# Optimization experiments

Hardware: AMD Instinct MI355X
Metric: run time of the kernel (lower is better)

Reference implementation:

```python
import jax, jax.numpy as jnp
import numpy as np

N, E, D, L, BOT = 50000, 800000, 64, 5, 15
EPS = 1e-5  # BatchNorm eps (torch default)
GATE = 0.01


def _bn(x, g, b):
    # training-mode BatchNorm1d over the node (batch) axis, biased variance
    m = jnp.mean(x, axis=0)
    v = jnp.mean((x - m) ** 2, axis=0)
    return (x - m) * jax.lax.rsqrt(v + EPS) * g + b


def _adapter(x, w1, b1, w2, b2, g, b):
    # Linear(D->BOT) -> ReLU -> Linear(BOT->D) -> BatchNorm1d
    h = jax.nn.relu(x @ w1 + b1)
    return _bn(h @ w2 + b2, g, b)


def setup_inputs() -> dict:
    key = jax.random.key(0)
    ks = jax.random.split(key, 8)
    x = jax.random.normal(ks[0], (N, D), dtype=jnp.float32)
    edge_index = jax.random.randint(ks[1], (2, E), 0, N, dtype=jnp.int32)
    # per-layer conv Linear weights
    W = jax.random.normal(ks[2], (L, D, D), dtype=jnp.float32) * 0.05
    b = jnp.zeros((L, D), dtype=jnp.float32)
    # per-layer output BatchNorm
    bn_g = jnp.ones((L, D), dtype=jnp.float32)
    bn_b = jnp.zeros((L, D), dtype=jnp.float32)
    # adapter branches: [prompt_num=2, L, ...] (random init so grads are nontrivial)
    pw1 = jax.random.normal(ks[3], (2, L, D, BOT), dtype=jnp.float32) * 0.1
    pb1 = jnp.zeros((2, L, BOT), dtype=jnp.float32)
    pw2 = jax.random.normal(ks[4], (2, L, BOT, D), dtype=jnp.float32) * 0.1
    pb2 = jnp.zeros((2, L, D), dtype=jnp.float32)
    pbn_g = jnp.ones((2, L, D), dtype=jnp.float32)
    pbn_b = jnp.zeros((2, L, D), dtype=jnp.float32)
    gating = jnp.full((2, L, 1), GATE, dtype=jnp.float32)
    return dict(x=x, edge_index=edge_index, W=W, b=b, bn_g=bn_g, bn_b=bn_b,
                pw1=pw1, pb1=pb1, pw2=pw2, pb2=pb2, pbn_g=pbn_g, pbn_b=pbn_b,
                gating=gating)


def reference(x, edge_index, W, b, bn_g, bn_b, pw1, pb1, pw2, pb2, pbn_g, pbn_b, gating):
    src, dst = edge_index[0], edge_index[1]
    h = x
    for l in range(L):
        # mess: sum-aggregate neighbor features (scatter-add over dst)
        x_aggr = jax.ops.segment_sum(h[src], dst, num_segments=N)  # [N, D]
        # conv: Linear on aggregated messages
        h_mlp = x_aggr @ W[l] + b[l]
        hn = _bn(h_mlp, bn_g[l], bn_b[l])
        # adapter branch 0 on layer input, branch 1 on aggregated messages
        hn = hn + _adapter(h, pw1[0, l], pb1[0, l], pw2[0, l], pb2[0, l], pbn_g[0, l], pbn_b[0, l]) * gating[0, l]
        hn = hn + _adapter(x_aggr, pw1[1, l], pb1[1, l], pw2[1, l], pb2[1, l], pbn_g[1, l], pbn_b[1, l]) * gating[1, l]
        if l < L - 1:
            hn = jax.nn.relu(hn)
        # dropout with drop_ratio=0 is a no-op
        h = hn
    return h
```

## Files before the change

kernel.cpp:

```cpp
#include <hip/hip_runtime.h>
#include <hip/hip_fp16.h>

#define DIM 64
#define BOT 15
#define NLAYERS 5
#define BN_EPS 1e-5f
#define ROWS 64
#define ROWS_FB 32
#define BKT_SHIFT 8
#define NSTRIPE 4

__device__ inline void fma4(float4& acc, const float4& a, float s) {
    acc.x = fmaf(a.x, s, acc.x); acc.y = fmaf(a.y, s, acc.y);
    acc.z = fmaf(a.z, s, acc.z); acc.w = fmaf(a.w, s, acc.w);
}
__device__ inline void add4(float4& acc, const float4& a) {
    acc.x += a.x; acc.y += a.y; acc.z += a.z; acc.w += a.w;
}
__device__ inline void fma4sq(float4& acc, const float4& a) {
    acc.x = fmaf(a.x, a.x, acc.x); acc.y = fmaf(a.y, a.y, acc.y);
    acc.z = fmaf(a.z, a.z, acc.z); acc.w = fmaf(a.w, a.w, acc.w);
}
__device__ inline void wavered4(float4& v) {
    v.x += __shfl_xor(v.x, 16); v.y += __shfl_xor(v.y, 16);
    v.z += __shfl_xor(v.z, 16); v.w += __shfl_xor(v.w, 16);
    v.x += __shfl_xor(v.x, 32); v.y += __shfl_xor(v.y, 32);
    v.z += __shfl_xor(v.z, 32); v.w += __shfl_xor(v.w, 32);
}


__global__ __launch_bounds__(256) void hist_k(const int* __restrict__ dst,
                                              int* __restrict__ deg, int E) {
    int e = blockIdx.x * blockDim.x + threadIdx.x;
    if (e < E) atomicAdd(&deg[dst[e]], 1);
}

__global__ __launch_bounds__(1024) void scan_part_k(const int* __restrict__ deg,
                                                    int* __restrict__ excl,
                                                    int* __restrict__ bsum, int n) {
    __shared__ int buf[1024];
    int t = threadIdx.x;
    int idx = blockIdx.x * 1024 + t;
    int v = (idx < n) ? deg[idx] : 0;
    buf[t] = v;
    __syncthreads();
    for (int off = 1; off < 1024; off <<= 1) {
        int x = (t >= off) ? buf[t - off] : 0;
        __syncthreads();
        buf[t] += x;
        __syncthreads();
    }
    if (idx < n) excl[idx] = buf[t] - v;
    if (t == 0) bsum[blockIdx.x] = buf[1023];
}

__global__ __launch_bounds__(1024) void scan_top_k(const int* __restrict__ bsum,
                                                   int* __restrict__ boff, int nb,
                                                   int* __restrict__ row_ptr, int n) {
    __shared__ int buf[1024];
    int t = threadIdx.x;
    int v = (t < nb) ? bsum[t] : 0;
    buf[t] = v;
    __syncthreads();
    for (int off = 1; off < 1024; off <<= 1) {
        int x = (t >= off) ? buf[t - off] : 0;
        __syncthreads();
        buf[t] += x;
        __syncthreads();
    }
    if (t < nb) boff[t] = buf[t] - v;
    if (t == 1023) row_ptr[n] = buf[1023];
}

__global__ __launch_bounds__(256) void scan_add_k(int* __restrict__ row_ptr,
                                                  const int* __restrict__ boff,
                                                  int* __restrict__ deg,
                                                  int* __restrict__ bcur, int n) {
    int i = blockIdx.x * blockDim.x + threadIdx.x;
    if (i < n) {
        int v = row_ptr[i] + boff[i >> 10];
        row_ptr[i] = v;
        deg[i] = v;
        if ((i & 255) == 0) bcur[i >> BKT_SHIFT] = v;
    }
}

__global__ __launch_bounds__(256) void scatter_k(const int* __restrict__ src,
                                                 const int* __restrict__ dst,
                                                 int* __restrict__ cursor,
                                                 int* __restrict__ csr, int E) {
    int e = blockIdx.x * blockDim.x + threadIdx.x;
    if (e < E) {
        int p = atomicAdd(&cursor[dst[e]], 1);
        csr[p] = src[e];
    }
}

__global__ __launch_bounds__(256) void part_k(const int* __restrict__ src,
                                              const int* __restrict__ dst,
                                              int* __restrict__ bcur,
                                              int2* __restrict__ part, int E) {
    __shared__ int hist[256];
    __shared__ int cur[256];
    int t = threadIdx.x;
    int base = blockIdx.x * 2048;
    hist[t] = 0;
    __syncthreads();
    int2 ed[8];
    int bk[8];
    #pragma unroll
    for (int k = 0; k < 8; k++) {
        int i = base + k * 256 + t;
        if (i < E) {
            ed[k].x = src[i];
            ed[k].y = dst[i];
            bk[k] = ed[k].y >> BKT_SHIFT;
            atomicAdd(&hist[bk[k]], 1);
        } else bk[k] = -1;
    }
    __syncthreads();
    int h = hist[t];
    if (h > 0) cur[t] = atomicAdd(&bcur[t], h);
    __syncthreads();
    #pragma unroll
    for (int k = 0; k < 8; k++) {
        if (bk[k] >= 0) {
            int p = atomicAdd(&cur[bk[k]], 1);
            part[p] = ed[k];
        }
    }
}

__global__ __launch_bounds__(256) void bscat_k(const int2* __restrict__ part,
                                               const int* __restrict__ row_ptr,
                                               int* __restrict__ cursor,
                                               int* __restrict__ csr, int n) {
    int b = blockIdx.x;
    int lo = row_ptr[b << BKT_SHIFT];
    int hiN = (b + 1) << BKT_SHIFT;
    int hi = row_ptr[hiN < n ? hiN : n];
    for (int i = lo + (int)threadIdx.x; i < hi; i += 256) {
        int2 e = part[i];
        int p = atomicAdd(&cursor[e.y], 1);
        csr[p] = e.x;
    }
}


__global__ __launch_bounds__(256) void tohalf_k(const float* __restrict__ x,
                                                __half* __restrict__ hh, int n4) {
    int i = blockIdx.x * blockDim.x + threadIdx.x;
    if (i >= n4) return;
    float4 v = *(const float4*)&x[(size_t)i * 4];
    __half2 a = __floats2half2_rn(v.x, v.y);
    __half2 b = __floats2half2_rn(v.z, v.w);
    uint2 pk;
    pk.x = *(unsigned int*)&a;
    pk.y = *(unsigned int*)&b;
    *(uint2*)&hh[(size_t)i * 4] = pk;
}


__global__ __launch_bounds__(256) void aggr_h_k(const __half* __restrict__ hh,
                                                const int* __restrict__ row_ptr,
                                                const int* __restrict__ csr,
                                                float* __restrict__ out, int n) {
    int gid = blockIdx.x * blockDim.x + threadIdx.x;
    int node = gid >> 6;
    int lane = threadIdx.x & 63;
    if (node >= n) return;
    int j = lane >> 3, q = lane & 7;
    int s = row_ptr[node], e = row_ptr[node + 1];
    float acc[8] = {0.f, 0.f, 0.f, 0.f, 0.f, 0.f, 0.f, 0.f};
    #pragma unroll 2
    for (int i = s; i < e; i += 8) {
        int ii = i + j;
        if (ii < e) {
            int idx = csr[ii];
            uint4 raw = *(const uint4*)&hh[(size_t)idx * DIM + q * 8];
            const __half2* hp = (const __half2*)&raw;
            #pragma unroll
            for (int k = 0; k < 4; k++) {
                acc[2 * k]     += __low2float(hp[k]);
                acc[2 * k + 1] += __high2float(hp[k]);
            }
        }
    }
    #pragma unroll
    for (int off = 8; off <= 32; off <<= 1) {
        #pragma unroll
        for (int k = 0; k < 8; k++) acc[k] += __shfl_xor(acc[k], off);
    }
    if (lane < 8) {
        float4 a = {acc[0], acc[1], acc[2], acc[3]};
        float4 b = {acc[4], acc[5], acc[6], acc[7]};
        *(float4*)&out[(size_t)node * DIM + q * 8] = a;
        *(float4*)&out[(size_t)node * DIM + q * 8 + 4] = b;
    }
}

__global__ __launch_bounds__(256) void aggr_k(const float* __restrict__ h,
                                              const int* __restrict__ row_ptr,
                                              const int* __restrict__ csr,
                                              float* __restrict__ out, int n) {
    int gid = blockIdx.x * blockDim.x + threadIdx.x;
    int node = gid >> 6;
    int lane = threadIdx.x & 63;
    if (node >= n) return;
    int j = lane >> 4, q = lane & 15;
    int s = row_ptr[node], e = row_ptr[node + 1];
    float4 acc = {0.f, 0.f, 0.f, 0.f};
    #pragma unroll 4
    for (int i = s; i < e; i += 4) {
        int ii = i + j;
        if (ii < e) {
            int idx = csr[ii];
            float4 v = *(const float4*)&h[(size_t)idx * DIM + q * 4];
            add4(acc, v);
        }
    }
    wavered4(acc);
    if (lane < 16) *(float4*)&out[(size_t)node * DIM + q * 4] = acc;
}


__global__ __launch_bounds__(512, 4) void stats_k(
    const float* __restrict__ h, const float* __restrict__ aggr,
    const float* __restrict__ Wc, const float* __restrict__ bc,
    const float* __restrict__ p1a, const float* __restrict__ b1a,
    const float* __restrict__ p2a, const float* __restrict__ b2a,
    const float* __restrict__ p1b, const float* __restrict__ b1b,
    const float* __restrict__ p2b, const float* __restrict__ b2b,
    float* __restrict__ gsum,
    float* __restrict__ yv, float* __restrict__ uv, float* __restrict__ vv,
    int n) {
    __shared__ float xa_s[ROWS][68];
    __shared__ float wc_s[64][64];
    __shared__ float p1t_s[2][15][68];
    __shared__ float p2_s[2][15][64];
    __shared__ float m_s[2][ROWS][17];
    __shared__ float red_s[6][8][64];

    int t = threadIdx.x;
    int rowBase = blockIdx.x * ROWS;

    #pragma unroll
    for (int i = 0; i < 2; i++) {
        int idx = t + i * 512;
        int r = idx >> 4, c4 = (idx & 15) * 4;
        int gr = rowBase + r;
        float4 va = {0.f, 0.f, 0.f, 0.f};
        if (gr < n) va = *(const float4*)&aggr[(size_t)gr * DIM + c4];
        *(float4*)&xa_s[r][c4] = va;
    }
    #pragma unroll
    for (int i = 0; i < 2; i++) {
        int idx = t + i * 512;
        int k = idx >> 4, c4 = (idx & 15) * 4;
        *(float4*)&wc_s[k][c4] = *(const float4*)&Wc[k * DIM + c4];
    }
    if (t < 240) {
        int m = t >> 4, c4 = (t & 15) * 4;
        *(float4*)&p2_s[0][m][c4] = *(const float4*)&p2a[m * DIM + c4];
        *(float4*)&p2_s[1][m][c4] = *(const float4*)&p2b[m * DIM + c4];
    }
    #pragma unroll
    for (int i = 0; i < 2; i++) {
        int idx = t + i * 512;
        if (idx < 960) {
            int k = idx / 15, m = idx % 15;
            p1t_s[0][m][k] = p1a[idx];
            p1t_s[1][m][k] = p1b[idx];
        }
    }
    __syncthreads();

    {
        int m = t & 15, r2 = t >> 4;
        if (m < 15) {
            #pragma unroll
            for (int half = 0; half < 2; half++) {
                int r = r2 + half * 32;
                int gr = rowBase + r;
                if (gr < n) {
                    float sA = b1a[m], sB = b1b[m];
                    const float4* hp = (const float4*)&h[(size_t)gr * DIM];
                    #pragma unroll 4
                    for (int kq = 0; kq < 16; kq++) {
                        float4 hv = hp[kq];
                        float4 av = *(const float4*)&xa_s[r][kq * 4];
                        float4 wA = *(const float4*)&p1t_s[0][m][kq * 4];
                        float4 wB = *(const float4*)&p1t_s[1][m][kq * 4];
                        sA = fmaf(hv.x, wA.x, sA); sA = fmaf(hv.y, wA.y, sA);
                        sA = fmaf(hv.z, wA.z, sA); sA = fmaf(hv.w, wA.w, sA);
                        sB = fmaf(av.x, wB.x, sB); sB = fmaf(av.y, wB.y, sB);
                        sB = fmaf(av.z, wB.z, sB); sB = fmaf(av.w, wB.w, sB);
                    }
                    m_s[0][r][m] = fmaxf(sA, 0.f);
                    m_s[1][r][m] = fmaxf(sB, 0.f);
                } else {
                    m_s[0][r][m] = 0.f;
                    m_s[1][r][m] = 0.f;
                }
            }
        }
    }
    __syncthreads();

    int cg = t & 15, rg = t >> 4;
    int c0 = cg * 4;
    int r0 = rg, r1 = rg + 32;

    float4 s0 = *(const float4*)&bc[c0];
    float4 s1 = s0;
    #pragma unroll 4
    for (int kq = 0; kq < 16; kq++) {
        float4 w0 = *(const float4*)&wc_s[kq * 4 + 0][c0];
        float4 w1 = *(const float4*)&wc_s[kq * 4 + 1][c0];
        float4 w2 = *(const float4*)&wc_s[kq * 4 + 2][c0];
        float4 w3 = *(const float4*)&wc_s[kq * 4 + 3][c0];
        float4 a0 = *(const float4*)&xa_s[r0][kq * 4];
        float4 a1 = *(const float4*)&xa_s[r1][kq * 4];
        fma4(s0, w0, a0.x); fma4(s0, w1, a0.y); fma4(s0, w2, a0.z); fma4(s0, w3, a0.w);
        fma4(s1, w0, a1.x); fma4(s1, w1, a1.y); fma4(s1, w2, a1.z); fma4(s1, w3, a1.w);
    }

    float4 u0 = *(const float4*)&b2a[c0];
    float4 u1 = u0;
    float4 v0 = *(const float4*)&b2b[c0];
    float4 v1 = v0;
    #pragma unroll 5
    for (int m = 0; m < BOT; m++) {
        float4 wa = *(const float4*)&p2_s[0][m][c0];
        float4 wb = *(const float4*)&p2_s[1][m][c0];
        float a0 = m_s[0][r0][m], a1 = m_s[0][r1][m];
        float b0 = m_s[1][r0][m], b1 = m_s[1][r1][m];
        fma4(u0, wa, a0); fma4(u1, wa, a1);
        fma4(v0, wb, b0); fma4(v1, wb, b1);
    }

    float4 sy = {0,0,0,0}, sy2 = {0,0,0,0};
    float4 su = {0,0,0,0}, su2 = {0,0,0,0};
    float4 sv = {0,0,0,0}, sv2 = {0,0,0,0};
    {
        int gr = rowBase + r0;
        if (gr < n) {
            size_t o = (size_t)gr * DIM + c0;
            *(float4*)&yv[o] = s0; *(float4*)&uv[o] = u0; *(float4*)&vv[o] = v0;
            add4(sy, s0); fma4sq(sy2, s0);
            add4(su, u0); fma4sq(su2, u0);
            add4(sv, v0); fma4sq(sv2, v0);
        }
        gr = rowBase + r1;
        if (gr < n) {
            size_t o = (size_t)gr * DIM + c0;
            *(float4*)&yv[o] = s1; *(float4*)&uv[o] = u1; *(float4*)&vv[o] = v1;
            add4(sy, s1); fma4sq(sy2, s1);
            add4(su, u1); fma4sq(su2, u1);
            add4(sv, v1); fma4sq(sv2, v1);
        }
    }

    wavered4(sy); wavered4(sy2);
    wavered4(su); wavered4(su2);
    wavered4(sv); wavered4(sv2);

    int wv = t >> 6, lane = t & 63;
    if (lane < 16) {
        *(float4*)&red_s[0][wv][c0] = sy;
        *(float4*)&red_s[1][wv][c0] = sy2;
        *(float4*)&red_s[2][wv][c0] = su;
        *(float4*)&red_s[3][wv][c0] = su2;
        *(float4*)&red_s[4][wv][c0] = sv;
        *(float4*)&red_s[5][wv][c0] = sv2;
    }
    __syncthreads();
    if (t < DIM) {
        float* gs = gsum + (size_t)(blockIdx.x & (NSTRIPE - 1)) * 6 * DIM;
        #pragma unroll
        for (int j = 0; j < 6; j++) {
            float v = red_s[j][0][t] + red_s[j][1][t] + red_s[j][2][t] + red_s[j][3][t]
                    + red_s[j][4][t] + red_s[j][5][t] + red_s[j][6][t] + red_s[j][7][t];
            atomicAdd(&gs[j * DIM + t], v);
        }
    }
}


template <int RELU, int WH>
__global__ __launch_bounds__(256) void apply_k(
    const float* __restrict__ yv, const float* __restrict__ uv,
    const float* __restrict__ vv, const float* __restrict__ gsum,
    const float* __restrict__ bn_g, const float* __restrict__ bn_b,
    const float* __restrict__ pg0, const float* __restrict__ pb0,
    const float* __restrict__ pg1, const float* __restrict__ pb1,
    const float* __restrict__ gating, int l, int n,
    float* __restrict__ out, __half* __restrict__ hh, int n4) {
    __shared__ float STs[6][64];
    int t = threadIdx.x;
    if (t < 192) {
        int stat = t >> 6, c = t & 63;
        float s1 = 0.f, s2 = 0.f;
        #pragma unroll
        for (int k = 0; k < NSTRIPE; k++) {
            const float* gs = gsum + (size_t)k * 6 * DIM;
            s1 += gs[(2 * stat) * DIM + c];
            s2 += gs[(2 * stat + 1) * DIM + c];
        }
        float mean = s1 / (float)n;
        float var = s2 / (float)n - mean * mean;
        float rstd = rsqrtf(fmaxf(var, 0.f) + BN_EPS);
        float g, bb, gate;
        if (stat == 0)      { g = bn_g[c]; bb = bn_b[c]; gate = 1.f; }
        else if (stat == 1) { g = pg0[c];  bb = pb0[c];  gate = gating[0 * NLAYERS + l]; }
        else                { g = pg1[c];  bb = pb1[c];  gate = gating[1 * NLAYERS + l]; }
        STs[2 * stat][c] = g * rstd * gate;
        STs[2 * stat + 1][c] = (bb - mean * g * rstd) * gate;
    }
    __syncthreads();
    int i = blockIdx.x * blockDim.x + t;
    if (i >= n4) return;
    int c4 = (i & 15) * 4;
    float4 S0 = *(const float4*)&STs[0][c4];
    float4 T0 = *(const float4*)&STs[1][c4];
    float4 S1 = *(const float4*)&STs[2][c4];
    float4 T1 = *(const float4*)&STs[3][c4];
    float4 S2 = *(const float4*)&STs[4][c4];
    float4 T2 = *(const float4*)&STs[5][c4];
    float4 y = *(const float4*)&yv[(size_t)i * 4];
    float4 u = *(const float4*)&uv[(size_t)i * 4];
    float4 v = *(const float4*)&vv[(size_t)i * 4];
    float4 r;
    r.x = fmaf(y.x, S0.x, T0.x) + fmaf(u.x, S1.x, T1.x) + fmaf(v.x, S2.x, T2.x);
    r.y = fmaf(y.y, S0.y, T0.y) + fmaf(u.y, S1.y, T1.y) + fmaf(v.y, S2.y, T2.y);
    r.z = fmaf(y.z, S0.z, T0.z) + fmaf(u.z, S1.z, T1.z) + fmaf(v.z, S2.z, T2.z);
    r.w = fmaf(y.w, S0.w, T0.w) + fmaf(u.w, S1.w, T1.w) + fmaf(v.w, S2.w, T2.w);
    if (RELU) {
        r.x = fmaxf(r.x, 0.f); r.y = fmaxf(r.y, 0.f);
        r.z = fmaxf(r.z, 0.f); r.w = fmaxf(r.w, 0.f);
    }
    *(float4*)&out[(size_t)i * 4] = r;
    if (WH) {
        __half2 a = __floats2half2_rn(r.x, r.y);
        __half2 b = __floats2half2_rn(r.z, r.w);
        uint2 pk;
        pk.x = *(unsigned int*)&a;
        pk.y = *(unsigned int*)&b;
        *(uint2*)&hh[(size_t)i * 4] = pk;
    }
}


template <int MODE>
__global__ __launch_bounds__(256) void layer_k(
    const float* __restrict__ h, const float* __restrict__ aggr,
    const float* __restrict__ Wc, const float* __restrict__ bc,
    const float* __restrict__ p1a, const float* __restrict__ b1a,
    const float* __restrict__ p2a, const float* __restrict__ b2a,
    const float* __restrict__ p1b, const float* __restrict__ b1b,
    const float* __restrict__ p2b, const float* __restrict__ b2b,
    float* __restrict__ partials, const float* __restrict__ ST,
    float* __restrict__ hout, int n) {
    __shared__ float xh[ROWS_FB][DIM + 1];
    __shared__ float xa[ROWS_FB][DIM + 1];
    __shared__ float m0[ROWS_FB][17];
    __shared__ float m1[ROWS_FB][17];
    __shared__ float red[6][4][DIM];

    int t = threadIdx.x;
    int rowBase = blockIdx.x * ROWS_FB;

    #pragma unroll
    for (int i = 0; i < (ROWS_FB * DIM) / 256; i++) {
        int idx = t + i * 256;
        int r = idx >> 6, c = idx & 63;
        int gr = rowBase + r;
        float vh = 0.f, va = 0.f;
        if (gr < n) { vh = h[(size_t)gr * DIM + c]; va = aggr[(size_t)gr * DIM + c]; }
        xh[r][c] = vh;
        xa[r][c] = va;
    }
    __syncthreads();

    {
        int r = t >> 3, sub = t & 7;
        #pragma unroll
        for (int half = 0; half < 2; half++) {
            int m = sub + half * 8;
            if (m < BOT) {
                float s0 = b1a[m], s1 = b1b[m];
                #pragma unroll
                for (int k = 0; k < DIM; k++) {
                    s0 = fmaf(xh[r][k], p1a[k * BOT + m], s0);
                    s1 = fmaf(xa[r][k], p1b[k * BOT + m], s1);
                }
                m0[r][m] = fmaxf(s0, 0.f);
                m1[r][m] = fmaxf(s1, 0.f);
            }
        }
    }
    __syncthreads();

    int col = t & 63;
    int rg = t >> 6;
    float sums[6] = {0.f, 0.f, 0.f, 0.f, 0.f, 0.f};
    float S0 = 0, T0 = 0, S1 = 0, T1 = 0, S2 = 0, T2 = 0;
    if (MODE != 0) {
        S0 = ST[col];        T0 = ST[64 + col];
        S1 = ST[128 + col];  T1 = ST[192 + col];
        S2 = ST[256 + col];  T2 = ST[320 + col];
    }
    #pragma unroll
    for (int i = 0; i < ROWS_FB / 4; i++) {
        int r = rg + i * 4;
        int gr = rowBase + r;
        float s = bc[col];
        #pragma unroll
        for (int k = 0; k < DIM; k++) s = fmaf(xa[r][k], Wc[k * DIM + col], s);
        float u = b2a[col];
        #pragma unroll
        for (int m = 0; m < BOT; m++) u = fmaf(m0[r][m], p2a[m * DIM + col], u);
        float v = b2b[col];
        #pragma unroll
        for (int m = 0; m < BOT; m++) v = fmaf(m1[r][m], p2b[m * DIM + col], v);
        if (MODE == 0) {
            if (gr < n) {
                sums[0] += s; sums[1] += s * s;
                sums[2] += u; sums[3] += u * u;
                sums[4] += v; sums[5] += v * v;
            }
        } else {
            float r0 = fmaf(s, S0, T0) + fmaf(u, S1, T1) + fmaf(v, S2, T2);
            if (MODE == 2) r0 = fmaxf(r0, 0.f);
            if (gr < n) hout[(size_t)gr * DIM + col] = r0;
        }
    }

    if (MODE == 0) {
        #pragma unroll
        for (int j = 0; j < 6; j++) red[j][rg][col] = sums[j];
        __syncthreads();
        if (t < DIM) {
            #pragma unroll
            for (int j = 0; j < 6; j++) {
                float v = red[j][0][t] + red[j][1][t] + red[j][2][t] + red[j][3][t];
                partials[((size_t)blockIdx.x * 6 + j) * DIM + t] = v;
            }
        }
    }
}


__global__ __launch_bounds__(256) void reduce_fold_k(
    const float* __restrict__ partials, int nb, int n,
    const float* __restrict__ bn_g, const float* __restrict__ bn_b,
    const float* __restrict__ pg0, const float* __restrict__ pb0,
    const float* __restrict__ pg1, const float* __restrict__ pb1,
    const float* __restrict__ gating, int l, float* __restrict__ ST) {
    __shared__ double red[6][256];
    int col = blockIdx.x;
    int t = threadIdx.x;
    double acc[6] = {0, 0, 0, 0, 0, 0};
    for (int b = t; b < nb; b += 256) {
        const float* p = partials + (size_t)b * 6 * DIM + col;
        #pragma unroll
        for (int j = 0; j < 6; j++) acc[j] += (double)p[j * DIM];
    }
    #pragma unroll
    for (int j = 0; j < 6; j++) red[j][t] = acc[j];
    __syncthreads();
    for (int off = 128; off > 0; off >>= 1) {
        if (t < off) {
            #pragma unroll
            for (int j = 0; j < 6; j++) red[j][t] += red[j][t + off];
        }
        __syncthreads();
    }
    if (t < 3) {
        int stat = t;
        float mean = (float)(red[2 * stat][0] / (double)n);
        float var = (float)(red[2 * stat + 1][0] / (double)n) - mean * mean;
        float rstd = rsqrtf(fmaxf(var, 0.f) + BN_EPS);
        float g, bb, gate;
        if (stat == 0)      { g = bn_g[col]; bb = bn_b[col]; gate = 1.f; }
        else if (stat == 1) { g = pg0[col];  bb = pb0[col];  gate = gating[0 * NLAYERS + l]; }
        else                { g = pg1[col];  bb = pb1[col];  gate = gating[1 * NLAYERS + l]; }
        float S = g * rstd * gate;
        float T = (bb - mean * g * rstd) * gate;
        ST[stat * 128 + col] = S;
        ST[stat * 128 + 64 + col] = T;
    }
}


static inline char* bump(char*& p, size_t bytes) {
    char* r = p;
    p += (bytes + 255) & ~(size_t)255;
    return r;
}

extern "C" void kernel_launch(void* const* d_in, const int* in_sizes, int n_in,
                              void* d_out, int out_size, void* d_ws, size_t ws_size,
                              hipStream_t stream) {
    const float* x      = (const float*)d_in[0];
    const int*   ei     = (const int*)d_in[1];
    const float* W      = (const float*)d_in[2];
    const float* bconv  = (const float*)d_in[3];
    const float* bn_g   = (const float*)d_in[4];
    const float* bn_b   = (const float*)d_in[5];
    const float* pw1    = (const float*)d_in[6];
    const float* pb1    = (const float*)d_in[7];
    const float* pw2    = (const float*)d_in[8];
    const float* pb2    = (const float*)d_in[9];
    const float* pbn_g  = (const float*)d_in[10];
    const float* pbn_b  = (const float*)d_in[11];
    const float* gating = (const float*)d_in[12];

    int n = in_sizes[0] / DIM;
    int E = in_sizes[1] / 2;
    int nbS  = (n + ROWS - 1) / ROWS;
    int nbFB = (n + ROWS_FB - 1) / ROWS_FB;
    int nb1024 = (n + 1023) / 1024;
    int nbkt = (n + 255) >> BKT_SHIFT;
    size_t n64b = (size_t)n * DIM * sizeof(float);
    int n4 = n * (DIM / 4);

    char* p = (char*)d_ws;
    float* h_ws     = (float*)bump(p, n64b);
    float* partials = (float*)bump(p, (size_t)nbFB * 6 * DIM * sizeof(float));
    float* ST       = (float*)bump(p, 6 * 128 * sizeof(float));
    float* gsum     = (float*)bump(p, (size_t)NLAYERS * NSTRIPE * 6 * DIM * sizeof(float));
    int*   bsum     = (int*)bump(p, (size_t)nb1024 * sizeof(int));
    int*   boff     = (int*)bump(p, (size_t)nb1024 * sizeof(int));
    int*   bcur     = (int*)bump(p, 257 * sizeof(int));
    int*   deg      = (int*)bump(p, (size_t)n * sizeof(int));
    int*   row_ptr  = (int*)bump(p, (size_t)(n + 1) * sizeof(int));
    int*   csr      = (int*)bump(p, (size_t)E * sizeof(int));
    float* aggr     = (float*)bump(p, n64b);
    float* yv = (float*)bump(p, n64b);
    float* uv = (float*)bump(p, n64b);
    float* vv = (float*)bump(p, n64b);
    __half* hh = (__half*)bump(p, (size_t)n * DIM * sizeof(__half));
    bool fast = ((size_t)(p - (char*)d_ws) <= ws_size);
    int2* part = (int2*)yv;

    const int* esrc = ei;
    const int* edst = ei + E;

    hipMemsetAsync(deg, 0, (size_t)n * sizeof(int), stream);
    hipMemsetAsync(gsum, 0, (size_t)NLAYERS * NSTRIPE * 6 * DIM * sizeof(float), stream);
    hist_k<<<(E + 255) / 256, 256, 0, stream>>>(edst, deg, E);
    scan_part_k<<<nb1024, 1024, 0, stream>>>(deg, row_ptr, bsum, n);
    scan_top_k<<<1, 1024, 0, stream>>>(bsum, boff, nb1024, row_ptr, n);
    scan_add_k<<<(n + 255) / 256, 256, 0, stream>>>(row_ptr, boff, deg, bcur, n);
    if (fast) {
        part_k<<<(E + 2047) / 2048, 256, 0, stream>>>(esrc, edst, bcur, part, E);
        bscat_k<<<nbkt, 256, 0, stream>>>(part, row_ptr, deg, csr, n);
        tohalf_k<<<(n4 + 255) / 256, 256, 0, stream>>>(x, hh, n4);
    } else {
        scatter_k<<<(E + 255) / 256, 256, 0, stream>>>(esrc, edst, deg, csr, E);
    }

    for (int l = 0; l < NLAYERS; l++) {
        const float* Wl  = W     + (size_t)l * DIM * DIM;
        const float* bl  = bconv + (size_t)l * DIM;
        const float* bgl = bn_g  + (size_t)l * DIM;
        const float* bbl = bn_b  + (size_t)l * DIM;
        const float* p1a = pw1 + ((size_t)0 * NLAYERS + l) * DIM * BOT;
        const float* p1b = pw1 + ((size_t)1 * NLAYERS + l) * DIM * BOT;
        const float* b1a = pb1 + ((size_t)0 * NLAYERS + l) * BOT;
        const float* b1b = pb1 + ((size_t)1 * NLAYERS + l) * BOT;
        const float* p2a = pw2 + ((size_t)0 * NLAYERS + l) * BOT * DIM;
        const float* p2b = pw2 + ((size_t)1 * NLAYERS + l) * BOT * DIM;
        const float* b2a = pb2 + ((size_t)0 * NLAYERS + l) * DIM;
        const float* b2b = pb2 + ((size_t)1 * NLAYERS + l) * DIM;
        const float* g0  = pbn_g + ((size_t)0 * NLAYERS + l) * DIM;
        const float* g1  = pbn_g + ((size_t)1 * NLAYERS + l) * DIM;
        const float* be0 = pbn_b + ((size_t)0 * NLAYERS + l) * DIM;
        const float* be1 = pbn_b + ((size_t)1 * NLAYERS + l) * DIM;

        const float* hin = (l == 0) ? x : h_ws;
        float* gsl = gsum + (size_t)l * NSTRIPE * 6 * DIM;

        if (fast) {
            aggr_h_k<<<(n + 3) / 4, 256, 0, stream>>>(hh, row_ptr, csr, aggr, n);

            stats_k<<<nbS, 512, 0, stream>>>(
                hin, aggr, Wl, bl, p1a, b1a, p2a, b2a,
                p1b, b1b, p2b, b2b, gsl, yv, uv, vv, n);

            float* outp = (l < NLAYERS - 1) ? h_ws : (float*)d_out;
            if (l < NLAYERS - 1)
                apply_k<1, 1><<<(n4 + 255) / 256, 256, 0, stream>>>(
                    yv, uv, vv, gsl, bgl, bbl, g0, be0, g1, be1, gating, l, n,
                    outp, hh, n4);
            else
                apply_k<0, 0><<<(n4 + 255) / 256, 256, 0, stream>>>(
                    yv, uv, vv, gsl, bgl, bbl, g0, be0, g1, be1, gating, l, n,
                    outp, hh, n4);
        } else {
            aggr_k<<<(n + 3) / 4, 256, 0, stream>>>(hin, row_ptr, csr, aggr, n);

            layer_k<0><<<nbFB, 256, 0, stream>>>(
                hin, aggr, Wl, bl, p1a, b1a, p2a, b2a, p1b, b1b, p2b, b2b,
                partials, nullptr, nullptr, n);

            reduce_fold_k<<<DIM, 256, 0, stream>>>(partials, nbFB, n, bgl, bbl,
                                                   g0, be0, g1, be1, gating, l, ST);

            if (l < NLAYERS - 1) {
                layer_k<2><<<nbFB, 256, 0, stream>>>(
                    hin, aggr, Wl, bl, p1a, b1a, p2a, b2a, p1b, b1b, p2b, b2b,
                    nullptr, ST, h_ws, n);
            } else {
                layer_k<1><<<nbFB, 256, 0, stream>>>(
                    hin, aggr, Wl, bl, p1a, b1a, p2a, b2a, p1b, b1b, p2b, b2b,
                    nullptr, ST, (float*)d_out, n);
            }
        }
    }
}
```

Measured before the change: 416.1 us.

## Store adapter outputs and layer input in fp16 to cut memory traffic

The stats kernel now reads the layer input from the fp16 copy instead of the fp32 buffer, and it writes the two adapter branch outputs (u, v) as fp16 rather than fp32. The apply kernel reads u/v as fp16 and, for non-final layers, writes only the fp16 hidden state, dropping the fp32 h_ws write. The aim is to shrink global memory traffic in these bandwidth-bound per-layer kernels. The cost is extra rounding of the layer input and the adapter outputs. The adapter outputs are scaled by the small gating factor, which limits the effect of that rounding.

```diff
diff --git a/kernel.cpp b/kernel.cpp
--- a/kernel.cpp
+++ b/kernel.cpp
@@ -26,6 +26,22 @@
     v.z += __shfl_xor(v.z, 16); v.w += __shfl_xor(v.w, 16);
     v.x += __shfl_xor(v.x, 32); v.y += __shfl_xor(v.y, 32);
     v.z += __shfl_xor(v.z, 32); v.w += __shfl_xor(v.w, 32);
+}
+__device__ inline uint2 packh4(const float4& v) {
+    __half2 a = __floats2half2_rn(v.x, v.y);
+    __half2 b = __floats2half2_rn(v.z, v.w);
+    uint2 pk;
+    pk.x = *(unsigned int*)&a;
+    pk.y = *(unsigned int*)&b;
+    return pk;
+}
+__device__ inline float4 unpackh4(uint2 pk) {
+    __half2 a = *(__half2*)&pk.x;
+    __half2 b = *(__half2*)&pk.y;
+    float4 v;
+    v.x = __low2float(a); v.y = __high2float(a);
+    v.z = __low2float(b); v.w = __high2float(b);
+    return v;
 }
 
 
@@ -152,12 +168,7 @@
     int i = blockIdx.x * blockDim.x + threadIdx.x;
     if (i >= n4) return;
     float4 v = *(const float4*)&x[(size_t)i * 4];
-    __half2 a = __floats2half2_rn(v.x, v.y);
-    __half2 b = __floats2half2_rn(v.z, v.w);
-    uint2 pk;
-    pk.x = *(unsigned int*)&a;
-    pk.y = *(unsigned int*)&b;
-    *(uint2*)&hh[(size_t)i * 4] = pk;
+    *(uint2*)&hh[(size_t)i * 4] = packh4(v);
 }
 
 
@@ -225,14 +236,14 @@
 
 
 __global__ __launch_bounds__(512, 4) void stats_k(
-    const float* __restrict__ h, const float* __restrict__ aggr,
+    const __half* __restrict__ hh, const float* __restrict__ aggr,
     const float* __restrict__ Wc, const float* __restrict__ bc,
     const float* __restrict__ p1a, const float* __restrict__ b1a,
     const float* __restrict__ p2a, const float* __restrict__ b2a,
     const float* __restrict__ p1b, const float* __restrict__ b1b,
     const float* __restrict__ p2b, const float* __restrict__ b2b,
     float* __restrict__ gsum,
-    float* __restrict__ yv, float* __restrict__ uv, float* __restrict__ vv,
+    float* __restrict__ yv, __half* __restrict__ uh, __half* __restrict__ vh,
     int n) {
     __shared__ float xa_s[ROWS][68];
     __shared__ float wc_s[64][64];
@@ -284,10 +295,10 @@
                 int gr = rowBase + r;
                 if (gr < n) {
                     float sA = b1a[m], sB = b1b[m];
-                    const float4* hp = (const float4*)&h[(size_t)gr * DIM];
+                    const uint2* hp = (const uint2*)&hh[(size_t)gr * DIM];
                     #pragma unroll 4
                     for (int kq = 0; kq < 16; kq++) {
-                        float4 hv = hp[kq];
+                        float4 hv = unpackh4(hp[kq]);
                         float4 av = *(const float4*)&xa_s[r][kq * 4];
                         float4 wA = *(const float4*)&p1t_s[0][m][kq * 4];
                         float4 wB = *(const float4*)&p1t_s[1][m][kq * 4];
@@ -346,7 +357,9 @@
         int gr = rowBase + r0;
         if (gr < n) {
             size_t o = (size_t)gr * DIM + c0;
-            *(float4*)&yv[o] = s0; *(float4*)&uv[o] = u0; *(float4*)&vv[o] = v0;
+            *(float4*)&yv[o] = s0;
+            *(uint2*)&uh[o] = packh4(u0);
+            *(uint2*)&vh[o] = packh4(v0);
             add4(sy, s0); fma4sq(sy2, s0);
             add4(su, u0); fma4sq(su2, u0);
             add4(sv, v0); fma4sq(sv2, v0);
@@ -354,7 +367,9 @@
         gr = rowBase + r1;
         if (gr < n) {
             size_t o = (size_t)gr * DIM + c0;
-            *(float4*)&yv[o] = s1; *(float4*)&uv[o] = u1; *(float4*)&vv[o] = v1;
+            *(float4*)&yv[o] = s1;
+            *(uint2*)&uh[o] = packh4(u1);
+            *(uint2*)&vh[o] = packh4(v1);
             add4(sy, s1); fma4sq(sy2, s1);
             add4(su, u1); fma4sq(su2, u1);
             add4(sv, v1); fma4sq(sv2, v1);
@@ -387,10 +402,10 @@
 }
 
 
-template <int RELU, int WH>
+template <int LAST>
 __global__ __launch_bounds__(256) void apply_k(
-    const float* __restrict__ yv, const float* __restrict__ uv,
-    const float* __restrict__ vv, const float* __restrict__ gsum,
+    const float* __restrict__ yv, const __half* __restrict__ uh,
+    const __half* __restrict__ vh, const float* __restrict__ gsum,
     const float* __restrict__ bn_g, const float* __restrict__ bn_b,
     const float* __restrict__ pg0, const float* __restrict__ pb0,
     const float* __restrict__ pg1, const float* __restrict__ pb1,
@@ -428,25 +443,19 @@
     float4 S2 = *(const float4*)&STs[4][c4];
     float4 T2 = *(const float4*)&STs[5][c4];
     float4 y = *(const float4*)&yv[(size_t)i * 4];
-    float4 u = *(const float4*)&uv[(size_t)i * 4];
-    float4 v = *(const float4*)&vv[(size_t)i * 4];
+    float4 u = unpackh4(*(const uint2*)&uh[(size_t)i * 4]);
+    float4 v = unpackh4(*(const uint2*)&vh[(size_t)i * 4]);
     float4 r;
     r.x = fmaf(y.x, S0.x, T0.x) + fmaf(u.x, S1.x, T1.x) + fmaf(v.x, S2.x, T2.x);
     r.y = fmaf(y.y, S0.y, T0.y) + fmaf(u.y, S1.y, T1.y) + fmaf(v.y, S2.y, T2.y);
     r.z = fmaf(y.z, S0.z, T0.z) + fmaf(u.z, S1.z, T1.z) + fmaf(v.z, S2.z, T2.z);
     r.w = fmaf(y.w, S0.w, T0.w) + fmaf(u.w, S1.w, T1.w) + fmaf(v.w, S2.w, T2.w);
-    if (RELU) {
+    if (!LAST) {
         r.x = fmaxf(r.x, 0.f); r.y = fmaxf(r.y, 0.f);
         r.z = fmaxf(r.z, 0.f); r.w = fmaxf(r.w, 0.f);
-    }
-    *(float4*)&out[(size_t)i * 4] = r;
-    if (WH) {
-        __half2 a = __floats2half2_rn(r.x, r.y);
-        __half2 b = __floats2half2_rn(r.z, r.w);
-        uint2 pk;
-        pk.x = *(unsigned int*)&a;
-        pk.y = *(unsigned int*)&b;
-        *(uint2*)&hh[(size_t)i * 4] = pk;
+        *(uint2*)&hh[(size_t)i * 4] = packh4(r);
+    } else {
+        *(float4*)&out[(size_t)i * 4] = r;
     }
 }
 
@@ -475,9 +484,9 @@
         int idx = t + i * 256;
         int r = idx >> 6, c = idx & 63;
         int gr = rowBase + r;
-        float vh = 0.f, va = 0.f;
-        if (gr < n) { vh = h[(size_t)gr * DIM + c]; va = aggr[(size_t)gr * DIM + c]; }
-        xh[r][c] = vh;
+        float vh2 = 0.f, va = 0.f;
+        if (gr < n) { vh2 = h[(size_t)gr * DIM + c]; va = aggr[(size_t)gr * DIM + c]; }
+        xh[r][c] = vh2;
         xa[r][c] = va;
     }
     __syncthreads();
@@ -623,6 +632,7 @@
     int nb1024 = (n + 1023) / 1024;
     int nbkt = (n + 255) >> BKT_SHIFT;
     size_t n64b = (size_t)n * DIM * sizeof(float);
+    size_t n64h = (size_t)n * DIM * sizeof(__half);
     int n4 = n * (DIM / 4);
 
     char* p = (char*)d_ws;
@@ -637,10 +647,10 @@
     int*   row_ptr  = (int*)bump(p, (size_t)(n + 1) * sizeof(int));
     int*   csr      = (int*)bump(p, (size_t)E * sizeof(int));
     float* aggr     = (float*)bump(p, n64b);
-    float* yv = (float*)bump(p, n64b);
-    float* uv = (float*)bump(p, n64b);
-    float* vv = (float*)bump(p, n64b);
-    __half* hh = (__half*)bump(p, (size_t)n * DIM * sizeof(__half));
+    float* yv  = (float*)bump(p, n64b);
+    __half* uh = (__half*)bump(p, n64h);
+    __half* vh = (__half*)bump(p, n64h);
+    __half* hh = (__half*)bump(p, n64h);
     bool fast = ((size_t)(p - (char*)d_ws) <= ws_size);
     int2* part = (int2*)yv;
 
@@ -679,26 +689,26 @@
         const float* be0 = pbn_b + ((size_t)0 * NLAYERS + l) * DIM;
         const float* be1 = pbn_b + ((size_t)1 * NLAYERS + l) * DIM;
 
-        const float* hin = (l == 0) ? x : h_ws;
         float* gsl = gsum + (size_t)l * NSTRIPE * 6 * DIM;
 
         if (fast) {
             aggr_h_k<<<(n + 3) / 4, 256, 0, stream>>>(hh, row_ptr, csr, aggr, n);
 
             stats_k<<<nbS, 512, 0, stream>>>(
-                hin, aggr, Wl, bl, p1a, b1a, p2a, b2a,
-                p1b, b1b, p2b, b2b, gsl, yv, uv, vv, n);
-
-            float* outp = (l < NLAYERS - 1) ? h_ws : (float*)d_out;
+                hh, aggr, Wl, bl, p1a, b1a, p2a, b2a,
+                p1b, b1b, p2b, b2b, gsl, yv, uh, vh, n);
+
             if (l < NLAYERS - 1)
-                apply_k<1, 1><<<(n4 + 255) / 256, 256, 0, stream>>>(
-                    yv, uv, vv, gsl, bgl, bbl, g0, be0, g1, be1, gating, l, n,
-                    outp, hh, n4);
+                apply_k<0><<<(n4 + 255) / 256, 256, 0, stream>>>(
+                    yv, uh, vh, gsl, bgl, bbl, g0, be0, g1, be1, gating, l, n,
+                    nullptr, hh, n4);
             else
-                apply_k<0, 0><<<(n4 + 255) / 256, 256, 0, stream>>>(
-                    yv, uv, vv, gsl, bgl, bbl, g0, be0, g1, be1, gating, l, n,
-                    outp, hh, n4);
+                apply_k<1><<<(n4 + 255) / 256, 256, 0, stream>>>(
+                    yv, uh, vh, gsl, bgl, bbl, g0, be0, g1, be1, gating, l, n,
+                    (float*)d_out, hh, n4);
         } else {
+            const float* hin = (l == 0) ? x : h_ws;
+
             aggr_k<<<(n + 3) / 4, 256, 0, stream>>>(hin, row_ptr, csr, aggr, n);
 
             layer_k<0><<<nbFB, 256, 0, stream>>>(
```

New measurement: 403.6 us. 1.03x faster.
